# Performance work log

Measured on AMD Instinct MI355X. Metric: run time of the kernel, lower is better.

The kernel has to match this reference:

```python
import jax, jax.numpy as jnp
import numpy as np
import math
from jax.scipy.special import gammaln

B, H, W = 32, 960, 960
BLOCK = 96  # official NIQE/NRQM block size

# AGGD shape-parameter lookup table (same grid as torch impl: 0.2..10 step 0.001)
_GAM_NP = np.arange(0.2, 10.0 + 1e-6, 0.001, dtype=np.float64)
_RG_NP = np.array([math.exp(2.0 * math.lgamma(2.0 / g) - math.lgamma(1.0 / g) - math.lgamma(3.0 / g)) for g in _GAM_NP], dtype=np.float32)
GAM = jnp.asarray(_GAM_NP.astype(np.float32))
RGAM = jnp.asarray(_RG_NP)

def _gauss_kernel(size, sigma):
    ax = np.arange(size, dtype=np.float64) - (size - 1) / 2.0
    xx, yy = np.meshgrid(ax, ax)
    k = np.exp(-(xx ** 2 + yy ** 2) / (2.0 * sigma ** 2))
    return (k / k.sum()).astype(np.float32)

K7 = jnp.asarray(_gauss_kernel(7, 7.0 / 6.0))[None, None]  # MSCN window
K3 = jnp.asarray(_gauss_kernel(3, 0.5))[None, None]        # pyramid / downsample kernel

def _conv_same(x, k, edge_pad):
    ph = k.shape[-1] // 2
    mode = 'edge' if edge_pad else 'constant'
    x = jnp.pad(x, ((0, 0), (0, 0), (ph, ph), (ph, ph)), mode=mode)
    return jax.lax.conv_general_dilated(x, k, (1, 1), 'VALID', dimension_numbers=('NCHW', 'OIHW', 'NCHW'))

def _normalize(img):
    # MSCN: (img - mu) / (sigma + 1), replicate padding
    mu = _conv_same(img, K7, True)
    sigma = jnp.sqrt(jnp.abs(_conv_same(img * img, K7, True) - mu * mu))
    return (img - mu) / (sigma + 1.0)

def _downsample(img):
    # gaussian blur (3x3, sigma 0.5, zero same-pad) + stride-2 decimation
    return _conv_same(img, K3, False)[:, :, ::2, ::2]

def _aggd(x):
    # x: [b, nb, h, w]; vectorized AGGD parameter estimation over all blocks
    hw = (-2, -1)
    x2 = x * x
    ml = (x < 0).astype(x.dtype)
    mr = (x > 0).astype(x.dtype)
    cl = jnp.maximum(ml.sum(hw), 1.0)
    cr = jnp.maximum(mr.sum(hw), 1.0)
    lstd = jnp.sqrt((x2 * ml).sum(hw) / cl)
    rstd = jnp.sqrt((x2 * mr).sum(hw) / cr)
    gh = lstd / jnp.maximum(rstd, 1e-12)
    rhat = jnp.mean(jnp.abs(x), hw) ** 2 / jnp.maximum(jnp.mean(x2, hw), 1e-12)
    rhn = rhat * (gh ** 3 + 1.0) * (gh + 1.0) / ((gh * gh + 1.0) ** 2)
    idx = jnp.argmin(jnp.abs(RGAM - rhn[..., None]), axis=-1)  # table lookup
    alpha = GAM[idx]
    conv = jnp.exp(0.5 * (gammaln(1.0 / alpha) - gammaln(3.0 / alpha)))
    return alpha, lstd * conv, rstd * conv

def _features(blocks):
    # 18 features per block: AGGD of block + AGGD of 4 shifted products
    alpha, bl, br = _aggd(blocks)
    feats = [alpha, (bl + br) / 2.0]
    for shift in ((0, 1), (1, 0), (1, 1), (1, -1)):
        sb = jnp.roll(blocks, shift, axis=(2, 3))
        a, l, r = _aggd(blocks * sb)
        mean = (r - l) * jnp.exp(gammaln(2.0 / a) - gammaln(1.0 / a))
        feats += [a, mean, l, r]
    return jnp.stack(feats, axis=-1)  # [b, nb, 18]

def _blocks(x, bs):
    b, _, h, w = x.shape
    nh, nw = h // bs, w // bs
    x = x[:, 0].reshape(b, nh, bs, nw, bs).transpose(0, 1, 3, 2, 4)
    return x.reshape(b, nh * nw, bs, bs)

def setup_inputs() -> dict:
    key = jax.random.key(0)
    k1, k2, k3 = jax.random.split(key, 3)
    X = jax.random.uniform(k1, (B, 1, H, W), jnp.float32) * 255.0
    mu_pris = jax.random.normal(k2, (36,), jnp.float32)
    A = jax.random.normal(k3, (36, 36), jnp.float32)
    cov_pris = A @ A.T / 36.0 + jnp.eye(36, dtype=jnp.float32)  # SPD pristine covariance
    return {"X": X, "mu_pris": mu_pris, "cov_pris": cov_pris}

def reference(X, mu_pris, cov_pris):
    feats = []
    img = X
    for scale in (1, 2):
        xn = _normalize(img)
        feats.append(_features(_blocks(xn, BLOCK // scale)))  # [b, 100, 18]
        if scale == 1:
            img = _downsample(img)
    d = jnp.concatenate(feats, axis=-1)  # [b, nb, 36]
    mu_dist = d.mean(axis=1)  # [b, 36]
    c = d - mu_dist[:, None, :]
    cov_dist = jnp.einsum('bnf,bng->bfg', c, c) / (d.shape[1] - 1)
    invcov = jnp.linalg.pinv((cov_pris[None] + cov_dist) / 2.0)
    diff = mu_pris[None] - mu_dist
    q = jnp.einsum('bf,bfg,bg->b', diff, invcov, diff)
    return jnp.sqrt(jnp.maximum(q, 0.0))
```

## Files before the change

### kernel.cpp

```cpp
#include <hip/hip_runtime.h>
#include <hip/hip_fp16.h>
#include <math.h>

#define NTAB 9801
typedef unsigned int uint;
typedef float f2v __attribute__((ext_vector_type(2)));
typedef _Float16 h2v __attribute__((ext_vector_type(2)));

struct WParams { float w1[7]; float wd[3]; };

__device__ inline __half2 u2h2(uint u) { return __builtin_bit_cast(__half2, u); }
__device__ inline float flo(uint u) { return __low2float(u2h2(u)); }
__device__ inline float fhi(uint u) { return __high2float(u2h2(u)); }
__device__ inline uint pkmul(uint a, uint b) { return __builtin_bit_cast(uint, __hmul2(u2h2(a), u2h2(b))); }
__device__ inline uint pack2(float a, float b) {
    return __builtin_bit_cast(uint, __builtin_amdgcn_cvt_pkrtz(a, b));
}
__device__ inline uint algn16(uint hi, uint lo) {
    return (uint)((((unsigned long long)hi << 32) | lo) >> 16);
}
__device__ inline float fdot2f(uint a, uint b, float c) {
    return __builtin_amdgcn_fdot2(__builtin_bit_cast(h2v, a), __builtin_bit_cast(h2v, b), c, false);
}
__device__ inline float rcpf(float x) { return __builtin_amdgcn_rcpf(x); }

__global__ __launch_bounds__(256) void tables_k(float* __restrict__ rgam) {
    int i = blockIdx.x * 256 + threadIdx.x;
    if (i >= NTAB) return;
    double g = 0.2 + (double)i * 0.001;
    rgam[i] = (float)exp(2.0 * lgamma(2.0 / g) - lgamma(1.0 / g) - lgamma(3.0 / g));
}

template <int CW, int TW, int NG, int RPG, int ORR>
__device__ __forceinline__ void mscn_tile(const uint* tin, uint* xs,
                                          const float* w1, int tid) {
    constexpr int TAIL = ORR - (NG - 1) * RPG;
    constexpr int LASTROW = ORR + 5;
    const int g = tid / CW, c = tid - g * CW;
    const int R0 = g * RPG;

    uint wA[4], wB[4];
    wA[0] = pack2(0.f, w1[0]);   wA[1] = pack2(w1[1], w1[2]);
    wA[2] = pack2(w1[3], w1[4]); wA[3] = pack2(w1[5], w1[6]);
    wB[0] = pack2(w1[0], w1[1]); wB[1] = pack2(w1[2], w1[3]);
    wB[2] = pack2(w1[4], w1[5]); wB[3] = pack2(w1[6], 0.f);

    auto mathq = [&](const uint* q, f2v& o1, f2v& o2) {
        uint p0 = pkmul(q[0], q[0]), p1 = pkmul(q[1], q[1]), p2 = pkmul(q[2], q[2]),
             p3 = pkmul(q[3], q[3]), p4 = pkmul(q[4], q[4]);
        float s1A = fdot2f(q[3], wA[3], fdot2f(q[2], wA[2], fdot2f(q[1], wA[1], fdot2f(q[0], wA[0], 0.f))));
        float s2A = fdot2f(p3, wA[3], fdot2f(p2, wA[2], fdot2f(p1, wA[1], fdot2f(p0, wA[0], 0.f))));
        float s1B = fdot2f(q[4], wB[3], fdot2f(q[3], wB[2], fdot2f(q[2], wB[1], fdot2f(q[1], wB[0], 0.f))));
        float s2B = fdot2f(p4, wB[3], fdot2f(p3, wB[2], fdot2f(p2, wB[1], fdot2f(p1, wB[0], 0.f))));
        o1 = (f2v){s1A, s1B};
        o2 = (f2v){s2A, s2B};
    };

    f2v r1[7], r2[7];
    uint cq[7];
    uint qcur0, qcur1, qcur2, qcur3, qcur4;

#pragma unroll
    for (int ir = 0; ir < 6; ir++) {
        const uint* pw = &tin[(R0 + ir) * TW + c];
        uint qq[5] = {pw[0], pw[1], pw[2], pw[3], pw[4]};
        mathq(qq, r1[ir], r2[ir]);
        cq[ir] = qq[2];
    }
    {
        const uint* pw = &tin[(R0 + 6) * TW + c];
        qcur0 = pw[0]; qcur1 = pw[1]; qcur2 = pw[2]; qcur3 = pw[3]; qcur4 = pw[4];
    }

#define MSCN_STEP(u)                                                          \
    {                                                                         \
        int nrow = R0 + (u) + 7; if (nrow > LASTROW) nrow = LASTROW;          \
        const uint* pw = &tin[nrow * TW + c];                                 \
        uint qn0 = pw[0], qn1 = pw[1], qn2 = pw[2], qn3 = pw[3], qn4 = pw[4]; \
        uint qq[5] = {qcur0, qcur1, qcur2, qcur3, qcur4};                     \
        mathq(qq, r1[((u) + 6) % 7], r2[((u) + 6) % 7]);                      \
        cq[((u) + 6) % 7] = qcur2;                                            \
        f2v a1 = (f2v)(0.f), a2 = (f2v)(0.f);                                 \
        _Pragma("unroll")                                                     \
        for (int dy = 0; dy < 7; dy++) {                                      \
            a1 += r1[((u) + dy) % 7] * w1[dy];                                \
            a2 += r2[((u) + dy) % 7] * w1[dy];                                \
        }                                                                     \
        uint qc = cq[((u) + 3) % 7];                                          \
        float v0a = flo(qc), v0b = fhi(qc);                                   \
        float xa = (v0a - a1.x) * rcpf(sqrtf(fabsf(a2.x - a1.x * a1.x)) + 1.f);\
        float xb = (v0b - a1.y) * rcpf(sqrtf(fabsf(a2.y - a1.y * a1.y)) + 1.f);\
        xs[(R0 + (u)) * CW + c] = pack2(xa, xb);                              \
        qcur0 = qn0; qcur1 = qn1; qcur2 = qn2; qcur3 = qn3; qcur4 = qn4;      \
    }

#pragma unroll
    for (int u = 0; u < TAIL; u++) MSCN_STEP(u)
    if constexpr (TAIL < RPG) {
        if (g < NG - 1) {
#pragma unroll
            for (int u = TAIL; u < RPG; u++) MSCN_STEP(u)
        }
    }
#undef MSCN_STEP
}

template <int BS, int NTHR>
__device__ __forceinline__ void feat_core(const uint* xs, float* red, float* tot,
                                          int b, int blk,
                                          const float* __restrict__ rgam,
                                          float* __restrict__ dfeat, int foff) {
    constexpr int WROW = BS / 2;
    constexpr int QUADS = BS * BS / 8;
    constexpr int QPR = WROW / 4;
    constexpr int NWAVE = NTHR / 64;
    constexpr int KMAX = (QUADS + NTHR - 1) / NTHR;
    const int tid = threadIdx.x;

    float ssq[5], sab[5], ssg[5];
    uint  cnt[5];
#pragma unroll
    for (int v = 0; v < 5; v++) { ssq[v] = sab[v] = ssg[v] = 0.f; cnt[v] = 0u; }

    const uint ONE2 = 0x3C003C00u;

    uint4 Vc, Ac; uint WLc, ALc, ARc;
    {
        int idx = tid;
        int y = idx / QPR, q = idx - y * QPR, w0 = q * 4;
        int rb = y * WROW, rbm = (y ? y - 1 : BS - 1) * WROW;
        Vc = *(const uint4*)&xs[rb + w0];
        Ac = *(const uint4*)&xs[rbm + w0];
        WLc = xs[rb  + (w0 ? w0 - 1 : WROW - 1)];
        ALc = xs[rbm + (w0 ? w0 - 1 : WROW - 1)];
        ARc = xs[rbm + ((w0 + 4 == WROW) ? 0 : w0 + 4)];
    }

#pragma unroll
    for (int k = 0; k < KMAX; k++) {
        uint4 Vn = Vc, An = Ac; uint WLn = WLc, ALn = ALc, ARn = ARc;
        int nidx = tid + (k + 1) * NTHR;
        if ((k + 1 < KMAX) && (nidx < QUADS)) {
            int y = nidx / QPR, q = nidx - y * QPR, w0 = q * 4;
            int rb = y * WROW, rbm = (y ? y - 1 : BS - 1) * WROW;
            Vn = *(const uint4*)&xs[rb + w0];
            An = *(const uint4*)&xs[rbm + w0];
            WLn = xs[rb  + (w0 ? w0 - 1 : WROW - 1)];
            ALn = xs[rbm + (w0 ? w0 - 1 : WROW - 1)];
            ARn = xs[rbm + ((w0 + 4 == WROW) ? 0 : w0 + 4)];
        }
        if (tid + k * NTHR < QUADS) {
            uint Vw[4] = {Vc.x, Vc.y, Vc.z, Vc.w};
            uint Aw[4] = {Ac.x, Ac.y, Ac.z, Ac.w};
            uint vprev = WLc, aprev = ALc;
#pragma unroll
            for (int j = 0; j < 4; j++) {
                uint anext = (j < 3) ? Aw[j + 1] : ARc;
                uint v0 = Vw[j];
                uint vv[5];
                vv[0] = v0;
                vv[1] = pkmul(v0, algn16(v0, vprev));
                vv[2] = pkmul(v0, Aw[j]);
                vv[3] = pkmul(v0, algn16(Aw[j], aprev));
                vv[4] = pkmul(v0, algn16(anext, Aw[j]));
#pragma unroll
                for (int v = 0; v < 5; v++) {
                    uint av = vv[v] & 0x7FFF7FFFu;
                    ssq[v] = fdot2f(vv[v], vv[v], ssq[v]);
                    sab[v] = fdot2f(av, ONE2, sab[v]);
                    ssg[v] = fdot2f(vv[v], av, ssg[v]);
                    cnt[v] += (vv[v] >> 15) & 0x00010001u;
                }
                vprev = v0; aprev = Aw[j];
            }
        }
        Vc = Vn; Ac = An; WLc = WLn; ALc = ALn; ARc = ARn;
    }

    const int wid = tid >> 6, lane = tid & 63;
#pragma unroll
    for (int v = 0; v < 5; v++) {
        float a = ssq[v], bb = sab[v], cc = ssg[v];
        float dd = (float)((cnt[v] & 0xFFFFu) + (cnt[v] >> 16));
        for (int off = 32; off >= 1; off >>= 1) {
            a += __shfl_down(a, off); bb += __shfl_down(bb, off);
            cc += __shfl_down(cc, off); dd += __shfl_down(dd, off);
        }
        if (lane == 0) {
            red[wid * 20 + v]      = a;
            red[wid * 20 + 5 + v]  = bb;
            red[wid * 20 + 10 + v] = cc;
            red[wid * 20 + 15 + v] = dd;
        }
    }
    __syncthreads();
    if (tid < 20) {
        float s = 0.f;
#pragma unroll
        for (int w = 0; w < NWAVE; w++) s += red[w * 20 + tid];
        tot[tid] = s;
    }
    __syncthreads();

    if (tid < 5) {
        const int v = tid;
        const float N = (float)(BS * BS);
        float ssqv = tot[v], sabv = tot[5 + v], ssgv = tot[10 + v], clv = tot[15 + v];
        float sql = fmaxf(0.5f * (ssqv - ssgv), 0.f);
        float sqr = fmaxf(0.5f * (ssqv + ssgv), 0.f);
        float cl = fmaxf(clv, 1.f), cr = fmaxf(N - clv, 1.f);
        float lstd = sqrtf(sql / cl), rstd = sqrtf(sqr / cr);
        float gh = lstd / fmaxf(rstd, 1e-12f);
        float mabs = sabv / N, msq = ssqv / N;
        float rhat = (mabs * mabs) / fmaxf(msq, 1e-12f);
        float gh2 = gh * gh;
        float target = rhat * (gh * gh2 + 1.f) * (gh + 1.f) / ((gh2 + 1.f) * (gh2 + 1.f));

        int lo = 0, hi = NTAB - 1, j = NTAB;
        while (lo <= hi) {
            int mid = (lo + hi) >> 1;
            if (rgam[mid] >= target) { j = mid; hi = mid - 1; } else lo = mid + 1;
        }
        int i0 = j > 0 ? j - 1 : 0;
        int i1 = j < NTAB ? j : NTAB - 1;
        float d0 = fabsf(rgam[i0] - target);
        float d1 = fabsf(rgam[i1] - target);
        int bi = (d1 < d0) ? i1 : i0;

        float alpha = (float)(0.2 + (double)bi * 0.001);
        float conv  = expf(0.5f * (lgammaf(1.f / alpha) - lgammaf(3.f / alpha)));
        float bl = lstd * conv, br = rstd * conv;
        float* outp = dfeat + ((size_t)b * 100 + blk) * 36 + foff;
        if (v == 0) {
            outp[0] = alpha;
            outp[1] = 0.5f * (bl + br);
        } else {
            float mean = (br - bl) * expf(lgammaf(2.f / alpha) - lgammaf(1.f / alpha));
            int base = 2 + (v - 1) * 4;
            outp[base + 0] = alpha; outp[base + 1] = mean;
            outp[base + 2] = bl;    outp[base + 3] = br;
        }
    }
}

__global__ __launch_bounds__(256, 5) void fused960_k(const float* __restrict__ X,
                                                     __half* __restrict__ img480,
                                                     const float* __restrict__ rgam,
                                                     float* __restrict__ dfeat,
                                                     WParams wp) {
    __shared__ __align__(16) uint tin[54 * 52];
    __shared__ __align__(16) uint xs[96 * 48];
    __shared__ float red[80];
    __shared__ float tot[20];

    const int tid = threadIdx.x;
    const int b   = blockIdx.x / 100;
    const int blk = blockIdx.x % 100;
    const int br  = blk / 10, bc = blk % 10;
    const int by  = br * 96, bx = bc * 96;

    const float* img = X + (size_t)b * 960 * 960;
    const bool interior = (br >= 1) && (br <= 8) && (bc >= 1) && (bc <= 8);
    const float* wd = wp.wd;

#pragma unroll
    for (int ph = 0; ph < 2; ph++) {
        if (ph) __syncthreads();
        const int ry0 = by + ph * 48 - 3;
        if (interior) {
            const float4* base = reinterpret_cast<const float4*>(
                img + (size_t)ry0 * 960 + (bx - 4));
            for (int i = tid; i < 26 * 54; i += 256) {
                int r = i / 26, k2 = i - r * 26;
                float4 v = base[(size_t)r * 240 + k2];
                uint2 pr2; pr2.x = pack2(v.x, v.y); pr2.y = pack2(v.z, v.w);
                *(uint2*)&tin[r * 52 + 2 * k2] = pr2;
            }
        } else {
            for (int i = tid; i < 54 * 52; i += 256) {
                int r = i / 52, w = i - r * 52;
                int gy = ry0 + r; gy = gy < 0 ? 0 : (gy > 959 ? 959 : gy);
                int c0 = bx - 4 + 2 * w; int c0c = c0 < 0 ? 0 : (c0 > 959 ? 959 : c0);
                int c1 = c0 + 1;         int c1c = c1 < 0 ? 0 : (c1 > 959 ? 959 : c1);
                const float* rp = img + (size_t)gy * 960;
                tin[i] = pack2(rp[c0c], rp[c1c]);
            }
        }
        __syncthreads();

        if (tid < 240) mscn_tile<48, 52, 5, 10, 48>(tin, xs + ph * 48 * 48, wp.w1, tid);

#pragma unroll
        for (int k = 0; k < 5; k++) {
            int o = tid + k * 256;
            if (o < 1152) {
                int j = ph * 24 + o / 48, d = o - (o / 48) * 48;
                int Yd = by / 2 + j, Xd = bx / 2 + d;
                float mL = (bx + 2 * d - 1 >= 0) ? 1.f : 0.f;
                float acc = 0.f;
#pragma unroll
                for (int a = 0; a < 3; a++) {
                    int gy = 2 * Yd - 1 + a;
                    if (gy < 0) continue;
                    int tr = gy - by - ph * 48 + 3;
                    uint u1 = tin[tr * 52 + d + 1];
                    uint u2 = tin[tr * 52 + d + 2];
                    acc += wd[a] * (wd[0] * fhi(u1) * mL + wd[1] * flo(u2) + wd[2] * fhi(u2));
                }
                img480[((size_t)b * 480 + Yd) * 480 + Xd] = __float2half(acc);
            }
        }
    }
    __syncthreads();

    feat_core<96, 256>(xs, red, tot, b, blk, rgam, dfeat, 0);
}

__global__ __launch_bounds__(256, 8) void fused480_k(const __half* __restrict__ img480,
                                                     const float* __restrict__ rgam,
                                                     float* __restrict__ dfeat,
                                                     WParams wp) {
    __shared__ __align__(16) uint tin[28 * 54];
    __shared__ __align__(16) uint xs[24 * 48];
    __shared__ float red[80];
    __shared__ float tot[20];

    const int tid = threadIdx.x;
    const int b   = blockIdx.x / 100;
    const int blk = blockIdx.x % 100;
    const int br  = blk / 10, bc = blk % 10;
    const int by  = br * 48, bx = bc * 48;

    const __half* img = img480 + (size_t)b * 480 * 480;
    const uint* gw = (const uint*)img;
    const bool interior = (br >= 1) && (br <= 8) && (bc >= 1) && (bc <= 8);

    if (interior) {
        for (int i = tid; i < 28 * 54; i += 256) {
            int r = i / 28, w = i - r * 28;
            tin[i] = gw[(((size_t)(by + r - 3) * 480 + (bx - 4)) >> 1) + w];
        }
    } else {
        for (int i = tid; i < 28 * 54; i += 256) {
            int r = i / 28, w = i - r * 28;
            int gy = by + r - 3; gy = gy < 0 ? 0 : (gy > 479 ? 479 : gy);
            int c0 = bx - 4 + 2 * w; int c0c = c0 < 0 ? 0 : (c0 > 479 ? 479 : c0);
            int c1 = c0 + 1;         int c1c = c1 < 0 ? 0 : (c1 > 479 ? 479 : c1);
            const __half* rp = img + (size_t)gy * 480;
            tin[i] = pack2(__half2float(rp[c0c]), __half2float(rp[c1c]));
        }
    }
    __syncthreads();

    if (tid < 192) mscn_tile<24, 28, 8, 6, 48>(tin, xs, wp.w1, tid);
    __syncthreads();

    feat_core<48, 256>(xs, red, tot, b, blk, rgam, dfeat, 18);
}

__global__ __launch_bounds__(256) void final_k(const float* __restrict__ dfeat,
                                               const float* __restrict__ mu_pris,
                                               const float* __restrict__ cov_pris,
                                               float* __restrict__ out) {
    __shared__ float  ds[3600];
    __shared__ float  mu[36];
    __shared__ double M[36][37];
    __shared__ double rhs[36];
    __shared__ double qacc;
    const int b = blockIdx.x, tid = threadIdx.x;
    const float* src = dfeat + (size_t)b * 3600;
    for (int i = tid; i < 3600; i += 256) ds[i] = src[i];
    __syncthreads();
    if (tid < 36) {
        float s = 0.f;
        for (int n = 0; n < 100; n++) s += ds[n * 36 + tid];
        mu[tid] = s / 100.f;
    }
    __syncthreads();
    for (int i = tid; i < 3600; i += 256) ds[i] -= mu[i % 36];
    if (tid < 36) rhs[tid] = (double)mu_pris[tid] - (double)mu[tid];
    if (tid == 0) qacc = 0.0;
    __syncthreads();
    for (int e = tid; e < 1296; e += 256) {
        int f = e / 36, g = e % 36;
        float s = 0.f;
        for (int n = 0; n < 100; n++) s += ds[n * 36 + f] * ds[n * 36 + g];
        M[f][g] = 0.5 * ((double)cov_pris[e] + (double)(s / 99.f));
    }
    __syncthreads();
    for (int j = 0; j < 36; j++) {
        if (tid == 0) qacc += rhs[j] * rhs[j] / M[j][j];
        int i = j + 1 + tid;
        if (i < 36) {
            double L = M[i][j] / M[j][j];
            for (int k = j; k < 36; k++) M[i][k] -= L * M[j][k];
            rhs[i] -= L * rhs[j];
        }
        __syncthreads();
    }
    if (tid == 0) out[b] = sqrtf((float)(qacc > 0.0 ? qacc : 0.0));
}

static WParams make_weights() {
    WParams p;
    double wt[7], s = 0.0; const double sg = 7.0 / 6.0;
    for (int i = 0; i < 7; i++) { double d = i - 3; wt[i] = exp(-d * d / (2.0 * sg * sg)); s += wt[i]; }
    for (int i = 0; i < 7; i++) p.w1[i] = (float)(wt[i] / s);
    double e1 = exp(-2.0), sd = 1.0 + 2.0 * e1;
    p.wd[0] = p.wd[2] = (float)(e1 / sd);
    p.wd[1] = (float)(1.0 / sd);
    return p;
}

extern "C" void kernel_launch(void* const* d_in, const int* in_sizes, int n_in,
                              void* d_out, int out_size, void* d_ws, size_t ws_size,
                              hipStream_t stream) {
    const float* X        = (const float*)d_in[0];
    const float* mu_pris  = (const float*)d_in[1];
    const float* cov_pris = (const float*)d_in[2];
    float* out = (float*)d_out;

    char* ws = (char*)d_ws;
    float*  rgam   = (float*)(ws);
    float*  dfeat  = (float*)(ws + 39424);
    __half* img480 = (__half*)(ws + 500224);

    WParams wp = make_weights();

    tables_k<<<(NTAB + 255) / 256, 256, 0, stream>>>(rgam);
    fused960_k<<<3200, 256, 0, stream>>>(X, img480, rgam, dfeat, wp);
    fused480_k<<<3200, 256, 0, stream>>>(img480, rgam, dfeat, wp);
    final_k<<<32, 256, 0, stream>>>(dfeat, mu_pris, cov_pris, out);
}
```

Baseline: 198.5 us.

## Compute 7x7 MSCN Gaussian window with MFMA banded matrix multiplies

The full-resolution kernel now loads the whole 112x120 tile into shared memory at once and expresses the separable 7-tap horizontal and vertical Gaussian passes for mu and E[x^2] as 16x16x32 fp16 MFMA products against banded weight matrices, with a transposed intermediate in shared memory. This replaces the per-thread dot2 sliding-window code. It also drops the two-phase loop and lowers the launch bound's blocks-per-SM hint because shared memory use is larger. The mscn_tile helper is simplified to reload rows from LDS instead of keeping them in registers. The aim is to move convolution arithmetic onto matrix cores, at the cost of more LDS, lower occupancy, and fp16 intermediate precision.

```diff
diff --git a/kernel.cpp b/kernel.cpp
--- a/kernel.cpp
+++ b/kernel.cpp
@@ -4,8 +4,11 @@
 
 #define NTAB 9801
 typedef unsigned int uint;
+typedef unsigned short ushort;
 typedef float f2v __attribute__((ext_vector_type(2)));
 typedef _Float16 h2v __attribute__((ext_vector_type(2)));
+typedef _Float16 f16x8 __attribute__((ext_vector_type(8)));
+typedef float f32x4 __attribute__((ext_vector_type(4)));
 
 struct WParams { float w1[7]; float wd[3]; };
 
@@ -35,7 +38,6 @@
 __device__ __forceinline__ void mscn_tile(const uint* tin, uint* xs,
                                           const float* w1, int tid) {
     constexpr int TAIL = ORR - (NG - 1) * RPG;
-    constexpr int LASTROW = ORR + 5;
     const int g = tid / CW, c = tid - g * CW;
     const int R0 = g * RPG;
 
@@ -45,53 +47,37 @@
     wB[0] = pack2(w1[0], w1[1]); wB[1] = pack2(w1[2], w1[3]);
     wB[2] = pack2(w1[4], w1[5]); wB[3] = pack2(w1[6], 0.f);
 
-    auto mathq = [&](const uint* q, f2v& o1, f2v& o2) {
-        uint p0 = pkmul(q[0], q[0]), p1 = pkmul(q[1], q[1]), p2 = pkmul(q[2], q[2]),
-             p3 = pkmul(q[3], q[3]), p4 = pkmul(q[4], q[4]);
-        float s1A = fdot2f(q[3], wA[3], fdot2f(q[2], wA[2], fdot2f(q[1], wA[1], fdot2f(q[0], wA[0], 0.f))));
+    auto horiz = [&](int row, f2v& o1, f2v& o2) {
+        const uint* pw = &tin[row * TW + c];
+        uint q0 = pw[0], q1 = pw[1], q2 = pw[2], q3 = pw[3], q4 = pw[4];
+        uint p0 = pkmul(q0, q0), p1 = pkmul(q1, q1), p2 = pkmul(q2, q2),
+             p3 = pkmul(q3, q3), p4 = pkmul(q4, q4);
+        float s1A = fdot2f(q3, wA[3], fdot2f(q2, wA[2], fdot2f(q1, wA[1], fdot2f(q0, wA[0], 0.f))));
         float s2A = fdot2f(p3, wA[3], fdot2f(p2, wA[2], fdot2f(p1, wA[1], fdot2f(p0, wA[0], 0.f))));
-        float s1B = fdot2f(q[4], wB[3], fdot2f(q[3], wB[2], fdot2f(q[2], wB[1], fdot2f(q[1], wB[0], 0.f))));
+        float s1B = fdot2f(q4, wB[3], fdot2f(q3, wB[2], fdot2f(q2, wB[1], fdot2f(q1, wB[0], 0.f))));
         float s2B = fdot2f(p4, wB[3], fdot2f(p3, wB[2], fdot2f(p2, wB[1], fdot2f(p1, wB[0], 0.f))));
         o1 = (f2v){s1A, s1B};
         o2 = (f2v){s2A, s2B};
     };
 
     f2v r1[7], r2[7];
-    uint cq[7];
-    uint qcur0, qcur1, qcur2, qcur3, qcur4;
-
-#pragma unroll
-    for (int ir = 0; ir < 6; ir++) {
-        const uint* pw = &tin[(R0 + ir) * TW + c];
-        uint qq[5] = {pw[0], pw[1], pw[2], pw[3], pw[4]};
-        mathq(qq, r1[ir], r2[ir]);
-        cq[ir] = qq[2];
-    }
-    {
-        const uint* pw = &tin[(R0 + 6) * TW + c];
-        qcur0 = pw[0]; qcur1 = pw[1]; qcur2 = pw[2]; qcur3 = pw[3]; qcur4 = pw[4];
-    }
+#pragma unroll
+    for (int ir = 0; ir < 6; ir++) horiz(R0 + ir, r1[ir], r2[ir]);
 
 #define MSCN_STEP(u)                                                          \
     {                                                                         \
-        int nrow = R0 + (u) + 7; if (nrow > LASTROW) nrow = LASTROW;          \
-        const uint* pw = &tin[nrow * TW + c];                                 \
-        uint qn0 = pw[0], qn1 = pw[1], qn2 = pw[2], qn3 = pw[3], qn4 = pw[4]; \
-        uint qq[5] = {qcur0, qcur1, qcur2, qcur3, qcur4};                     \
-        mathq(qq, r1[((u) + 6) % 7], r2[((u) + 6) % 7]);                      \
-        cq[((u) + 6) % 7] = qcur2;                                            \
+        horiz(R0 + (u) + 6, r1[((u) + 6) % 7], r2[((u) + 6) % 7]);            \
         f2v a1 = (f2v)(0.f), a2 = (f2v)(0.f);                                 \
         _Pragma("unroll")                                                     \
         for (int dy = 0; dy < 7; dy++) {                                      \
             a1 += r1[((u) + dy) % 7] * w1[dy];                                \
             a2 += r2[((u) + dy) % 7] * w1[dy];                                \
         }                                                                     \
-        uint qc = cq[((u) + 3) % 7];                                          \
+        uint qc = tin[(R0 + (u) + 3) * TW + c + 2];                           \
         float v0a = flo(qc), v0b = fhi(qc);                                   \
         float xa = (v0a - a1.x) * rcpf(sqrtf(fabsf(a2.x - a1.x * a1.x)) + 1.f);\
         float xb = (v0b - a1.y) * rcpf(sqrtf(fabsf(a2.y - a1.y * a1.y)) + 1.f);\
         xs[(R0 + (u)) * CW + c] = pack2(xa, xb);                              \
-        qcur0 = qn0; qcur1 = qn1; qcur2 = qn2; qcur3 = qn3; qcur4 = qn4;      \
     }
 
 #pragma unroll
@@ -243,13 +229,13 @@
     }
 }
 
-__global__ __launch_bounds__(256, 5) void fused960_k(const float* __restrict__ X,
+__global__ __launch_bounds__(256, 2) void fused960_k(const float* __restrict__ X,
                                                      __half* __restrict__ img480,
                                                      const float* __restrict__ rgam,
                                                      float* __restrict__ dfeat,
                                                      WParams wp) {
-    __shared__ __align__(16) uint tin[54 * 52];
-    __shared__ __align__(16) uint xs[96 * 48];
+    __shared__ __align__(16) _Float16 Xh[112 * 120];
+    __shared__ __align__(16) _Float16 Ht[2][96 * 120];
     __shared__ float red[80];
     __shared__ float tot[20];
 
@@ -258,43 +244,104 @@
     const int blk = blockIdx.x % 100;
     const int br  = blk / 10, bc = blk % 10;
     const int by  = br * 96, bx = bc * 96;
-
+    const int lane = tid & 63, wid = tid >> 6;
+    const float* w1 = wp.w1;
     const float* img = X + (size_t)b * 960 * 960;
+
     const bool interior = (br >= 1) && (br <= 8) && (bc >= 1) && (bc <= 8);
-    const float* wd = wp.wd;
-
-#pragma unroll
-    for (int ph = 0; ph < 2; ph++) {
-        if (ph) __syncthreads();
-        const int ry0 = by + ph * 48 - 3;
-        if (interior) {
-            const float4* base = reinterpret_cast<const float4*>(
-                img + (size_t)ry0 * 960 + (bx - 4));
-            for (int i = tid; i < 26 * 54; i += 256) {
-                int r = i / 26, k2 = i - r * 26;
-                float4 v = base[(size_t)r * 240 + k2];
-                uint2 pr2; pr2.x = pack2(v.x, v.y); pr2.y = pack2(v.z, v.w);
-                *(uint2*)&tin[r * 52 + 2 * k2] = pr2;
-            }
-        } else {
-            for (int i = tid; i < 54 * 52; i += 256) {
-                int r = i / 52, w = i - r * 52;
-                int gy = ry0 + r; gy = gy < 0 ? 0 : (gy > 959 ? 959 : gy);
-                int c0 = bx - 4 + 2 * w; int c0c = c0 < 0 ? 0 : (c0 > 959 ? 959 : c0);
-                int c1 = c0 + 1;         int c1c = c1 < 0 ? 0 : (c1 > 959 ? 959 : c1);
-                const float* rp = img + (size_t)gy * 960;
-                tin[i] = pack2(rp[c0c], rp[c1c]);
-            }
-        }
-        __syncthreads();
-
-        if (tid < 240) mscn_tile<48, 52, 5, 10, 48>(tin, xs + ph * 48 * 48, wp.w1, tid);
-
-#pragma unroll
-        for (int k = 0; k < 5; k++) {
+    if (interior) {
+        const float4* base = (const float4*)(img + (size_t)(by - 3) * 960 + (bx - 4));
+        for (int i = tid; i < 112 * 30; i += 256) {
+            int r = i / 30, k4 = i - r * 30;
+            float4 v = base[(size_t)r * 240 + k4];
+            uint2 pr; pr.x = pack2(v.x, v.y); pr.y = pack2(v.z, v.w);
+            *(uint2*)&Xh[r * 120 + 4 * k4] = pr;
+        }
+    } else {
+        uint* Xw = (uint*)Xh;
+        for (int i = tid; i < 112 * 60; i += 256) {
+            int r = i / 60, w = i - r * 60;
+            int gy = by - 3 + r; gy = gy < 0 ? 0 : (gy > 959 ? 959 : gy);
+            int c0 = bx - 4 + 2 * w; int c0c = c0 < 0 ? 0 : (c0 > 959 ? 959 : c0);
+            int c1 = c0 + 1;         int c1c = c1 < 0 ? 0 : (c1 > 959 ? 959 : c1);
+            const float* rp = img + (size_t)gy * 960;
+            Xw[r * 60 + w] = pack2(rp[c0c], rp[c1c]);
+        }
+    }
+
+    const int fn = lane & 15, kb = (lane >> 4) * 8;
+    f16x8 wH, wV;
+#pragma unroll
+    for (int i = 0; i < 8; i++) {
+        int dh = kb + i - fn - 1;
+        wH[i] = (dh >= 0 && dh < 7) ? (_Float16)w1[dh] : (_Float16)0.f;
+        int dv = kb + i - fn;
+        wV[i] = (dv >= 0 && dv < 7) ? (_Float16)w1[dv] : (_Float16)0.f;
+    }
+    __syncthreads();
+
+    for (int t = 0; t < 21; t++) {
+        int u = wid + t * 4;
+        int mt = u / 12, rest = u - mt * 12;
+        int nt = rest >> 1, sq = rest & 1;
+        int m0 = mt * 16, c0 = nt * 16;
+        f16x8 a = *(const f16x8*)&Xh[(m0 + fn) * 120 + c0 + kb];
+        if (sq) a = a * a;
+        f32x4 d = __builtin_amdgcn_mfma_f32_16x16x32_f16(
+            a, wH, (f32x4){0.f, 0.f, 0.f, 0.f}, 0, 0, 0);
+        uint2 pr; pr.x = pack2(d[0], d[1]); pr.y = pack2(d[2], d[3]);
+        *(uint2*)&Ht[sq][(c0 + fn) * 120 + m0 + (lane >> 4) * 4] = pr;
+    }
+    __syncthreads();
+
+    uint xnbuf[9][2];
+#pragma unroll
+    for (int t = 0; t < 9; t++) {
+        int u = wid + t * 4;
+        int rt = u / 6, nt = u - rt * 6;
+        int r0 = rt * 16, c0 = nt * 16;
+        f16x8 b1 = *(const f16x8*)&Ht[0][(c0 + fn) * 120 + r0 + kb];
+        f16x8 b2 = *(const f16x8*)&Ht[1][(c0 + fn) * 120 + r0 + kb];
+        f32x4 s1 = __builtin_amdgcn_mfma_f32_16x16x32_f16(
+            wV, b1, (f32x4){0.f, 0.f, 0.f, 0.f}, 0, 0, 0);
+        f32x4 s2 = __builtin_amdgcn_mfma_f32_16x16x32_f16(
+            wV, b2, (f32x4){0.f, 0.f, 0.f, 0.f}, 0, 0, 0);
+        float xv[4];
+#pragma unroll
+        for (int j = 0; j < 4; j++) {
+            int r = r0 + (lane >> 4) * 4 + j;
+            float v0 = (float)Xh[(r + 3) * 120 + c0 + fn + 4];
+            xv[j] = (v0 - s1[j]) * rcpf(sqrtf(fabsf(s2[j] - s1[j] * s1[j])) + 1.f);
+        }
+        xnbuf[t][0] = pack2(xv[0], xv[1]);
+        xnbuf[t][1] = pack2(xv[2], xv[3]);
+    }
+    __syncthreads();
+
+    ushort* xsh = (ushort*)&Ht[0][0];
+#pragma unroll
+    for (int t = 0; t < 9; t++) {
+        int u = wid + t * 4;
+        int rt = u / 6, nt = u - rt * 6;
+        int r0 = rt * 16, c0 = nt * 16;
+        uint wlo = xnbuf[t][0], whi = xnbuf[t][1];
+        ushort h0 = (ushort)(wlo & 0xFFFFu), h1 = (ushort)(wlo >> 16);
+        ushort h2 = (ushort)(whi & 0xFFFFu), h3 = (ushort)(whi >> 16);
+        int rb0 = r0 + (lane >> 4) * 4;
+        int cc = c0 + fn;
+        xsh[(rb0 + 0) * 96 + cc] = h0;
+        xsh[(rb0 + 1) * 96 + cc] = h1;
+        xsh[(rb0 + 2) * 96 + cc] = h2;
+        xsh[(rb0 + 3) * 96 + cc] = h3;
+    }
+    {
+        const float* wd = wp.wd;
+        const uint* Xw = (const uint*)Xh;
+#pragma unroll
+        for (int k = 0; k < 9; k++) {
             int o = tid + k * 256;
-            if (o < 1152) {
-                int j = ph * 24 + o / 48, d = o - (o / 48) * 48;
+            if (o < 2304) {
+                int j = o / 48, d = o - j * 48;
                 int Yd = by / 2 + j, Xd = bx / 2 + d;
                 float mL = (bx + 2 * d - 1 >= 0) ? 1.f : 0.f;
                 float acc = 0.f;
@@ -302,9 +349,9 @@
                 for (int a = 0; a < 3; a++) {
                     int gy = 2 * Yd - 1 + a;
                     if (gy < 0) continue;
-                    int tr = gy - by - ph * 48 + 3;
-                    uint u1 = tin[tr * 52 + d + 1];
-                    uint u2 = tin[tr * 52 + d + 2];
+                    int tr = gy - by + 3;
+                    uint u1 = Xw[tr * 60 + d + 1];
+                    uint u2 = Xw[tr * 60 + d + 2];
                     acc += wd[a] * (wd[0] * fhi(u1) * mL + wd[1] * flo(u2) + wd[2] * fhi(u2));
                 }
                 img480[((size_t)b * 480 + Yd) * 480 + Xd] = __float2half(acc);
@@ -313,7 +360,7 @@
     }
     __syncthreads();
 
-    feat_core<96, 256>(xs, red, tot, b, blk, rgam, dfeat, 0);
+    feat_core<96, 256>((const uint*)&Ht[0][0], red, tot, b, blk, rgam, dfeat, 0);
 }
 
 __global__ __launch_bounds__(256, 8) void fused480_k(const __half* __restrict__ img480,
```

Result: slower. 264.5 us (+33.2%).

## Merge both scale kernels into one launch, recomputing downsample from input

Applied to the files above, without the earlier changes.

Replaces the two per-scale kernels with one mega kernel whose blocks 0-3199 handle the 960 scale and the rest handle the 480 scale. The 480-scale blocks compute the 3x3 blurred, stride-2 downsample directly from the fp32 input instead of reading an fp16 intermediate image written by the first kernel. This removes the intermediate buffer round trip and the dependency between the two launches, so both scales can run concurrently. The cost is redundant global reads and arithmetic for the downsample. The MSCN tile code also stops software-pipelining its row loads and re-reads shared memory for each row instead, which cuts register pressure but adds LDS traffic.

```diff
diff --git a/kernel.cpp b/kernel.cpp
--- a/kernel.cpp
+++ b/kernel.cpp
@@ -35,7 +35,6 @@
 __device__ __forceinline__ void mscn_tile(const uint* tin, uint* xs,
                                           const float* w1, int tid) {
     constexpr int TAIL = ORR - (NG - 1) * RPG;
-    constexpr int LASTROW = ORR + 5;
     const int g = tid / CW, c = tid - g * CW;
     const int R0 = g * RPG;
 
@@ -45,53 +44,37 @@
     wB[0] = pack2(w1[0], w1[1]); wB[1] = pack2(w1[2], w1[3]);
     wB[2] = pack2(w1[4], w1[5]); wB[3] = pack2(w1[6], 0.f);
 
-    auto mathq = [&](const uint* q, f2v& o1, f2v& o2) {
-        uint p0 = pkmul(q[0], q[0]), p1 = pkmul(q[1], q[1]), p2 = pkmul(q[2], q[2]),
-             p3 = pkmul(q[3], q[3]), p4 = pkmul(q[4], q[4]);
-        float s1A = fdot2f(q[3], wA[3], fdot2f(q[2], wA[2], fdot2f(q[1], wA[1], fdot2f(q[0], wA[0], 0.f))));
+    auto horiz = [&](int row, f2v& o1, f2v& o2) {
+        const uint* pw = &tin[row * TW + c];
+        uint q0 = pw[0], q1 = pw[1], q2 = pw[2], q3 = pw[3], q4 = pw[4];
+        uint p0 = pkmul(q0, q0), p1 = pkmul(q1, q1), p2 = pkmul(q2, q2),
+             p3 = pkmul(q3, q3), p4 = pkmul(q4, q4);
+        float s1A = fdot2f(q3, wA[3], fdot2f(q2, wA[2], fdot2f(q1, wA[1], fdot2f(q0, wA[0], 0.f))));
         float s2A = fdot2f(p3, wA[3], fdot2f(p2, wA[2], fdot2f(p1, wA[1], fdot2f(p0, wA[0], 0.f))));
-        float s1B = fdot2f(q[4], wB[3], fdot2f(q[3], wB[2], fdot2f(q[2], wB[1], fdot2f(q[1], wB[0], 0.f))));
+        float s1B = fdot2f(q4, wB[3], fdot2f(q3, wB[2], fdot2f(q2, wB[1], fdot2f(q1, wB[0], 0.f))));
         float s2B = fdot2f(p4, wB[3], fdot2f(p3, wB[2], fdot2f(p2, wB[1], fdot2f(p1, wB[0], 0.f))));
         o1 = (f2v){s1A, s1B};
         o2 = (f2v){s2A, s2B};
     };
 
     f2v r1[7], r2[7];
-    uint cq[7];
-    uint qcur0, qcur1, qcur2, qcur3, qcur4;
-
-#pragma unroll
-    for (int ir = 0; ir < 6; ir++) {
-        const uint* pw = &tin[(R0 + ir) * TW + c];
-        uint qq[5] = {pw[0], pw[1], pw[2], pw[3], pw[4]};
-        mathq(qq, r1[ir], r2[ir]);
-        cq[ir] = qq[2];
-    }
-    {
-        const uint* pw = &tin[(R0 + 6) * TW + c];
-        qcur0 = pw[0]; qcur1 = pw[1]; qcur2 = pw[2]; qcur3 = pw[3]; qcur4 = pw[4];
-    }
+#pragma unroll
+    for (int ir = 0; ir < 6; ir++) horiz(R0 + ir, r1[ir], r2[ir]);
 
 #define MSCN_STEP(u)                                                          \
     {                                                                         \
-        int nrow = R0 + (u) + 7; if (nrow > LASTROW) nrow = LASTROW;          \
-        const uint* pw = &tin[nrow * TW + c];                                 \
-        uint qn0 = pw[0], qn1 = pw[1], qn2 = pw[2], qn3 = pw[3], qn4 = pw[4]; \
-        uint qq[5] = {qcur0, qcur1, qcur2, qcur3, qcur4};                     \
-        mathq(qq, r1[((u) + 6) % 7], r2[((u) + 6) % 7]);                      \
-        cq[((u) + 6) % 7] = qcur2;                                            \
+        horiz(R0 + (u) + 6, r1[((u) + 6) % 7], r2[((u) + 6) % 7]);            \
         f2v a1 = (f2v)(0.f), a2 = (f2v)(0.f);                                 \
         _Pragma("unroll")                                                     \
         for (int dy = 0; dy < 7; dy++) {                                      \
             a1 += r1[((u) + dy) % 7] * w1[dy];                                \
             a2 += r2[((u) + dy) % 7] * w1[dy];                                \
         }                                                                     \
-        uint qc = cq[((u) + 3) % 7];                                          \
+        uint qc = tin[(R0 + (u) + 3) * TW + c + 2];                           \
         float v0a = flo(qc), v0b = fhi(qc);                                   \
         float xa = (v0a - a1.x) * rcpf(sqrtf(fabsf(a2.x - a1.x * a1.x)) + 1.f);\
         float xb = (v0b - a1.y) * rcpf(sqrtf(fabsf(a2.y - a1.y * a1.y)) + 1.f);\
         xs[(R0 + (u)) * CW + c] = pack2(xa, xb);                              \
-        qcur0 = qn0; qcur1 = qn1; qcur2 = qn2; qcur3 = qn3; qcur4 = qn4;      \
     }
 
 #pragma unroll
@@ -243,119 +226,103 @@
     }
 }
 
-__global__ __launch_bounds__(256, 5) void fused960_k(const float* __restrict__ X,
-                                                     __half* __restrict__ img480,
-                                                     const float* __restrict__ rgam,
-                                                     float* __restrict__ dfeat,
-                                                     WParams wp) {
-    __shared__ __align__(16) uint tin[54 * 52];
-    __shared__ __align__(16) uint xs[96 * 48];
+#define NB960 3200
+#define NB480 3200
+#define SMEM_WORDS (54 * 52 + 96 * 48)
+
+__global__ __launch_bounds__(256, 5) void mega_k(const float* __restrict__ X,
+                                                 const float* __restrict__ rgam,
+                                                 float* __restrict__ dfeat,
+                                                 WParams wp) {
+    __shared__ __align__(16) uint smem[SMEM_WORDS];
     __shared__ float red[80];
     __shared__ float tot[20];
 
     const int tid = threadIdx.x;
-    const int b   = blockIdx.x / 100;
-    const int blk = blockIdx.x % 100;
-    const int br  = blk / 10, bc = blk % 10;
-    const int by  = br * 96, bx = bc * 96;
-
-    const float* img = X + (size_t)b * 960 * 960;
-    const bool interior = (br >= 1) && (br <= 8) && (bc >= 1) && (bc <= 8);
-    const float* wd = wp.wd;
-
-#pragma unroll
-    for (int ph = 0; ph < 2; ph++) {
-        if (ph) __syncthreads();
-        const int ry0 = by + ph * 48 - 3;
-        if (interior) {
-            const float4* base = reinterpret_cast<const float4*>(
-                img + (size_t)ry0 * 960 + (bx - 4));
-            for (int i = tid; i < 26 * 54; i += 256) {
-                int r = i / 26, k2 = i - r * 26;
-                float4 v = base[(size_t)r * 240 + k2];
-                uint2 pr2; pr2.x = pack2(v.x, v.y); pr2.y = pack2(v.z, v.w);
-                *(uint2*)&tin[r * 52 + 2 * k2] = pr2;
+    const int bid = blockIdx.x;
+
+    if (bid < NB960) {
+        uint* tin = smem;
+        uint* xs  = smem + 54 * 52;
+        const int b   = bid / 100;
+        const int blk = bid % 100;
+        const int br  = blk / 10, bc = blk % 10;
+        const int by  = br * 96, bx = bc * 96;
+
+        const float* img = X + (size_t)b * 960 * 960;
+        const bool interior = (br >= 1) && (br <= 8) && (bc >= 1) && (bc <= 8);
+
+#pragma unroll
+        for (int ph = 0; ph < 2; ph++) {
+            if (ph) __syncthreads();
+            const int ry0 = by + ph * 48 - 3;
+            if (interior) {
+                const float4* base = reinterpret_cast<const float4*>(
+                    img + (size_t)ry0 * 960 + (bx - 4));
+                for (int i = tid; i < 26 * 54; i += 256) {
+                    int r = i / 26, k2 = i - r * 26;
+                    float4 v = base[(size_t)r * 240 + k2];
+                    uint2 pr2; pr2.x = pack2(v.x, v.y); pr2.y = pack2(v.z, v.w);
+                    *(uint2*)&tin[r * 52 + 2 * k2] = pr2;
+                }
+            } else {
+                for (int i = tid; i < 54 * 52; i += 256) {
+                    int r = i / 52, w = i - r * 52;
+                    int gy = ry0 + r; gy = gy < 0 ? 0 : (gy > 959 ? 959 : gy);
+                    int c0 = bx - 4 + 2 * w; int c0c = c0 < 0 ? 0 : (c0 > 959 ? 959 : c0);
+                    int c1 = c0 + 1;         int c1c = c1 < 0 ? 0 : (c1 > 959 ? 959 : c1);
+                    const float* rp = img + (size_t)gy * 960;
+                    tin[i] = pack2(rp[c0c], rp[c1c]);
+                }
             }
-        } else {
-            for (int i = tid; i < 54 * 52; i += 256) {
-                int r = i / 52, w = i - r * 52;
-                int gy = ry0 + r; gy = gy < 0 ? 0 : (gy > 959 ? 959 : gy);
-                int c0 = bx - 4 + 2 * w; int c0c = c0 < 0 ? 0 : (c0 > 959 ? 959 : c0);
-                int c1 = c0 + 1;         int c1c = c1 < 0 ? 0 : (c1 > 959 ? 959 : c1);
-                const float* rp = img + (size_t)gy * 960;
-                tin[i] = pack2(rp[c0c], rp[c1c]);
+            __syncthreads();
+            if (tid < 240) mscn_tile<48, 52, 5, 10, 48>(tin, xs + ph * 48 * 48, wp.w1, tid);
+        }
+        __syncthreads();
+
+        feat_core<96, 256>(xs, red, tot, b, blk, rgam, dfeat, 0);
+    } else {
+        uint* dtin = smem;
+        uint* xs   = smem + 1512;
+        const int bid2 = bid - NB960;
+        const int b   = bid2 / 100;
+        const int blk = bid2 % 100;
+        const int br  = blk / 10, bc = blk % 10;
+        const int by  = br * 48, bx = bc * 48;
+
+        const float* img = X + (size_t)b * 960 * 960;
+        const float* wd = wp.wd;
+
+        for (int i = tid; i < 28 * 54; i += 256) {
+            int r = i / 28, w = i - (i / 28) * 28;
+            int Yc = by - 3 + r; Yc = Yc < 0 ? 0 : (Yc > 479 ? 479 : Yc);
+            float o0 = 0.f, o1 = 0.f;
+#pragma unroll
+            for (int e = 0; e < 2; e++) {
+                int Xcc = bx - 4 + 2 * w + e;
+                Xcc = Xcc < 0 ? 0 : (Xcc > 479 ? 479 : Xcc);
+                float acc = 0.f;
+#pragma unroll
+                for (int a = 0; a < 3; a++) {
+                    int gy = 2 * Yc - 1 + a;
+                    if (gy < 0) continue;
+                    const float* rp = img + (size_t)gy * 960;
+                    int gx = 2 * Xcc - 1;
+                    float rs = wd[1] * rp[gx + 1] + wd[2] * rp[gx + 2];
+                    if (gx >= 0) rs += wd[0] * rp[gx];
+                    acc += wd[a] * rs;
+                }
+                if (e == 0) o0 = acc; else o1 = acc;
             }
+            dtin[i] = pack2(o0, o1);
         }
         __syncthreads();
 
-        if (tid < 240) mscn_tile<48, 52, 5, 10, 48>(tin, xs + ph * 48 * 48, wp.w1, tid);
-
-#pragma unroll
-        for (int k = 0; k < 5; k++) {
-            int o = tid + k * 256;
-            if (o < 1152) {
-                int j = ph * 24 + o / 48, d = o - (o / 48) * 48;
-                int Yd = by / 2 + j, Xd = bx / 2 + d;
-                float mL = (bx + 2 * d - 1 >= 0) ? 1.f : 0.f;
-                float acc = 0.f;
-#pragma unroll
-                for (int a = 0; a < 3; a++) {
-                    int gy = 2 * Yd - 1 + a;
-                    if (gy < 0) continue;
-                    int tr = gy - by - ph * 48 + 3;
-                    uint u1 = tin[tr * 52 + d + 1];
-                    uint u2 = tin[tr * 52 + d + 2];
-                    acc += wd[a] * (wd[0] * fhi(u1) * mL + wd[1] * flo(u2) + wd[2] * fhi(u2));
-                }
-                img480[((size_t)b * 480 + Yd) * 480 + Xd] = __float2half(acc);
-            }
-        }
-    }
-    __syncthreads();
-
-    feat_core<96, 256>(xs, red, tot, b, blk, rgam, dfeat, 0);
-}
-
-__global__ __launch_bounds__(256, 8) void fused480_k(const __half* __restrict__ img480,
-                                                     const float* __restrict__ rgam,
-                                                     float* __restrict__ dfeat,
-                                                     WParams wp) {
-    __shared__ __align__(16) uint tin[28 * 54];
-    __shared__ __align__(16) uint xs[24 * 48];
-    __shared__ float red[80];
-    __shared__ float tot[20];
-
-    const int tid = threadIdx.x;
-    const int b   = blockIdx.x / 100;
-    const int blk = blockIdx.x % 100;
-    const int br  = blk / 10, bc = blk % 10;
-    const int by  = br * 48, bx = bc * 48;
-
-    const __half* img = img480 + (size_t)b * 480 * 480;
-    const uint* gw = (const uint*)img;
-    const bool interior = (br >= 1) && (br <= 8) && (bc >= 1) && (bc <= 8);
-
-    if (interior) {
-        for (int i = tid; i < 28 * 54; i += 256) {
-            int r = i / 28, w = i - r * 28;
-            tin[i] = gw[(((size_t)(by + r - 3) * 480 + (bx - 4)) >> 1) + w];
-        }
-    } else {
-        for (int i = tid; i < 28 * 54; i += 256) {
-            int r = i / 28, w = i - r * 28;
-            int gy = by + r - 3; gy = gy < 0 ? 0 : (gy > 479 ? 479 : gy);
-            int c0 = bx - 4 + 2 * w; int c0c = c0 < 0 ? 0 : (c0 > 479 ? 479 : c0);
-            int c1 = c0 + 1;         int c1c = c1 < 0 ? 0 : (c1 > 479 ? 479 : c1);
-            const __half* rp = img + (size_t)gy * 480;
-            tin[i] = pack2(__half2float(rp[c0c]), __half2float(rp[c1c]));
-        }
-    }
-    __syncthreads();
-
-    if (tid < 192) mscn_tile<24, 28, 8, 6, 48>(tin, xs, wp.w1, tid);
-    __syncthreads();
-
-    feat_core<48, 256>(xs, red, tot, b, blk, rgam, dfeat, 18);
+        if (tid < 192) mscn_tile<24, 28, 8, 6, 48>(dtin, xs, wp.w1, tid);
+        __syncthreads();
+
+        feat_core<48, 256>(xs, red, tot, b, blk, rgam, dfeat, 18);
+    }
 }
 
 __global__ __launch_bounds__(256) void final_k(const float* __restrict__ dfeat,
@@ -421,14 +388,12 @@
     float* out = (float*)d_out;
 
     char* ws = (char*)d_ws;
-    float*  rgam   = (float*)(ws);
-    float*  dfeat  = (float*)(ws + 39424);
-    __half* img480 = (__half*)(ws + 500224);
+    float*  rgam  = (float*)(ws);
+    float*  dfeat = (float*)(ws + 39424);
 
     WParams wp = make_weights();
 
     tables_k<<<(NTAB + 255) / 256, 256, 0, stream>>>(rgam);
-    fused960_k<<<3200, 256, 0, stream>>>(X, img480, rgam, dfeat, wp);
-    fused480_k<<<3200, 256, 0, stream>>>(img480, rgam, dfeat, wp);
+    mega_k<<<NB960 + NB480, 256, 0, stream>>>(X, rgam, dfeat, wp);
     final_k<<<32, 256, 0, stream>>>(dfeat, mu_pris, cov_pris, out);
 }
```

After: 228.1 us. +14.9%, slower.
